# Optimization experiments

Hardware: AMD Instinct MI355X
Metric: run time of the kernel (lower is better)

The kernel has to match this reference:

```python
import jax, jax.numpy as jnp
import numpy as np

NUM_CODES = 8192
DIM = 512
COMMITMENT_COST = 0.25


def setup_inputs() -> dict:
    key = jax.random.key(0)
    kx, kc = jax.random.split(key)
    x = jax.random.normal(kx, (8, 4096, DIM), dtype=jnp.float32)
    # nn.init.uniform_(codebook.weight, -1/num_codes, 1/num_codes)
    bound = 1.0 / NUM_CODES
    codebook = jax.random.uniform(kc, (NUM_CODES, DIM), dtype=jnp.float32,
                                  minval=-bound, maxval=bound)
    return {"x": x, "codebook": codebook}


def reference(x, codebook):
    orig_shape = x.shape
    flat = x.reshape(-1, orig_shape[-1])              # [N, D]
    # Squared-distance expansion (argmin-equivalent to torch.cdist's L2):
    # ||f||^2 - 2 f.c + ||c||^2
    x_sq = jnp.sum(flat * flat, axis=-1, keepdims=True)          # [N, 1]
    c_sq = jnp.sum(codebook * codebook, axis=-1)                 # [K]
    dists = x_sq - 2.0 * jnp.einsum('nd,kd->nk', flat, codebook) + c_sq  # [N, K]
    indices_flat = jnp.argmin(dists, axis=-1)                    # [N] int
    quantized_flat = codebook[indices_flat]                      # [N, D]
    # codebook_loss = mse(quantized, sg(flat)); commitment = mse(flat, sg(quantized))
    codebook_loss = jnp.mean((quantized_flat - jax.lax.stop_gradient(flat)) ** 2)
    commitment_loss = jnp.mean((flat - jax.lax.stop_gradient(quantized_flat)) ** 2)
    vq_loss = codebook_loss + COMMITMENT_COST * commitment_loss
    # straight-through
    quantized_st = flat + jax.lax.stop_gradient(quantized_flat - flat)
    return (quantized_st.reshape(orig_shape), vq_loss,
            indices_flat.reshape(orig_shape[:-1]))
```

## Files before the change

kernel.cpp:

```cpp
#include <hip/hip_runtime.h>


#define NROWS 32768
#define KCODES 8192
#define DD 512
#define CAP 24
#define MARGIN 2.5e-4f

typedef __bf16 bf16_t;
typedef __bf16 bf16x4 __attribute__((ext_vector_type(4)));
typedef __bf16 bf16x8 __attribute__((ext_vector_type(8)));
typedef float f32x4 __attribute__((ext_vector_type(4)));

__device__ __forceinline__ int lofs(int row, int s) {
  return row * 32 + (((s ^ ((row >> 1) & 3))) << 3);
}

__device__ __forceinline__ void gld16(const bf16_t* g, bf16_t* l) {
  __builtin_amdgcn_global_load_lds(
      (const __attribute__((address_space(1))) void*)g,
      (__attribute__((address_space(3))) void*)l, 16, 0, 0);
}

__global__ __launch_bounds__(256) void sumsq_kernel(const float* __restrict__ in,
                                                    float* __restrict__ out,
                                                    int nrows) {
  const int wave = threadIdx.x >> 6;
  const int lane = threadIdx.x & 63;
  const int row = blockIdx.x * 4 + wave;
  if (row >= nrows) return;
  const float* p = in + (size_t)row * DD;
  double s = 0.0;
#pragma unroll
  for (int j = 0; j < DD / 64; ++j) {
    float v = p[j * 64 + lane];
    float sq = v * v;
    s += (double)sq;
  }
  for (int off = 32; off > 0; off >>= 1) s += __shfl_down(s, off, 64);
  if (lane == 0) out[row] = (float)s;
}

__global__ __launch_bounds__(256) void cvt_kernel(const float* __restrict__ in,
                                                  bf16_t* __restrict__ outb) {
  const int t = blockIdx.x * 256 + threadIdx.x;
  float4 v = *(const float4*)(in + (size_t)t * 4);
  bf16x4 o = {(bf16_t)v.x, (bf16_t)v.y, (bf16_t)v.z, (bf16_t)v.w};
  *(bf16x4*)(outb + (size_t)t * 4) = o;
}

__global__ __launch_bounds__(256, 2) void coarse_kernel(
    const bf16_t* __restrict__ xbf, const bf16_t* __restrict__ cbbf,
    const float* __restrict__ csq, int* __restrict__ cnt_g,
    int* __restrict__ list_g) {
  __shared__ bf16_t As[128 * 32];
  __shared__ bf16_t Bs[256 * 32];
  __shared__ unsigned long long best[128];
  __shared__ int cnt_l[128];
  __shared__ int list_l[128 * CAP];

  const int tid = threadIdx.x;
  const int w = tid >> 6;
  const int lane = tid & 63;
  const int q = lane >> 4;
  const int l15 = lane & 15;
  const int rOff = (w & 1) * 64;
  const int cOff = (w >> 1) * 128;
  const int row0 = blockIdx.x * 128;
  const int cbase = blockIdx.y * (KCODES / 2);

  for (int i = tid; i < 128; i += 256) { best[i] = ~0ULL; cnt_l[i] = 0; }

  const int sub = lane >> 2;
  const int pos = lane & 3;
  int arowc[2];
  const bf16_t *agp[2];
  bf16_t *alp[2];
#pragma unroll
  for (int a = 0; a < 2; ++a) {
    const int row = w * 32 + a * 16 + sub;
    const int sg = pos ^ ((row >> 1) & 3);
    arowc[a] = row;
    agp[a] = xbf + (size_t)(row0 + row) * DD + sg * 8;
    alp[a] = As + row * 32 + pos * 8;
  }
  const bf16_t *bgp[4];
  bf16_t *blp[4];
#pragma unroll
  for (int b = 0; b < 4; ++b) {
    const int row = w * 64 + b * 16 + sub;
    const int sg = pos ^ ((row >> 1) & 3);
    bgp[b] = cbbf + (size_t)(cbase + row) * DD + sg * 8;
    blp[b] = Bs + row * 32 + pos * 8;
  }

  int afofs[4], bfofs[8];
#pragma unroll
  for (int rt = 0; rt < 4; ++rt) afofs[rt] = lofs(rOff + rt * 16 + l15, q);
#pragma unroll
  for (int ct = 0; ct < 8; ++ct) bfofs[ct] = lofs(cOff + ct * 16 + l15, q);

  __syncthreads();

#pragma unroll 1
  for (int ci = 0; ci < (KCODES / 2) / 256; ++ci) {
    const int c0 = cbase + ci * 256;
    const size_t coff = (size_t)(ci * 256) * DD;
    f32x4 acc[4][8];
#pragma unroll
    for (int rt = 0; rt < 4; ++rt)
#pragma unroll
      for (int ct = 0; ct < 8; ++ct) {
        f32x4 z = {0.f, 0.f, 0.f, 0.f};
        acc[rt][ct] = z;
      }

#pragma unroll 1
    for (int kc = 0; kc < DD / 32; ++kc) {
      const int kb = kc * 32;
      __syncthreads();
      gld16(agp[0] + kb, alp[0]);
      gld16(agp[1] + kb, alp[1]);
#pragma unroll
      for (int b = 0; b < 4; ++b) gld16(bgp[b] + coff + kb, blp[b]);
      __syncthreads();

      bf16x8 af[4], bfr[8];
#pragma unroll
      for (int rt = 0; rt < 4; ++rt) af[rt] = *(const bf16x8*)&As[afofs[rt]];
#pragma unroll
      for (int ct = 0; ct < 8; ++ct) bfr[ct] = *(const bf16x8*)&Bs[bfofs[ct]];
#pragma unroll
      for (int rt = 0; rt < 4; ++rt)
#pragma unroll
        for (int ct = 0; ct < 8; ++ct)
          acc[rt][ct] = __builtin_amdgcn_mfma_f32_16x16x32_bf16(
              af[rt], bfr[ct], acc[rt][ct], 0, 0, 0);
    }

    float cs1[8];
#pragma unroll
    for (int ct = 0; ct < 8; ++ct)
      cs1[ct] = 1.0f + csq[c0 + cOff + ct * 16 + l15];

#pragma unroll
    for (int rt = 0; rt < 4; ++rt) {
#pragma unroll
      for (int reg = 0; reg < 4; ++reg) {
        unsigned long long pk = ~0ULL;
#pragma unroll
        for (int ct = 0; ct < 8; ++ct) {
          float d = fmaf(-2.0f, acc[rt][ct][reg], cs1[ct]);
          unsigned long long p =
              ((unsigned long long)__float_as_uint(d) << 32) |
              (unsigned)(c0 + cOff + ct * 16 + l15);
          if (p < pk) pk = p;
        }
#pragma unroll
        for (int m = 1; m <= 8; m <<= 1) {
          unsigned long long o = __shfl_xor(pk, m, 64);
          if (o < pk) pk = o;
        }
        if (l15 == 0) atomicMin(&best[rOff + rt * 16 + q * 4 + reg], pk);
      }
    }
    __syncthreads();

#pragma unroll
    for (int rt = 0; rt < 4; ++rt) {
#pragma unroll
      for (int reg = 0; reg < 4; ++reg) {
        const int rloc = rOff + rt * 16 + q * 4 + reg;
        const float thr = __uint_as_float((unsigned)(best[rloc] >> 32)) + MARGIN;
#pragma unroll
        for (int ct = 0; ct < 8; ++ct) {
          float d = fmaf(-2.0f, acc[rt][ct][reg], cs1[ct]);
          if (d <= thr) {
            int pos2 = atomicAdd(&cnt_l[rloc], 1);
            if (pos2 < CAP)
              list_l[rloc * CAP + pos2] = c0 + cOff + ct * 16 + l15;
          }
        }
      }
    }
    __syncthreads();
  }

  const int half = blockIdx.y;
  for (int i = tid; i < 128; i += 256) cnt_g[(row0 + i) * 2 + half] = cnt_l[i];
  for (int i = tid; i < 128 * CAP; i += 256) {
    const int r = i / CAP, p = i % CAP;
    list_g[((size_t)(row0 + r) * 2 + half) * CAP + p] = list_l[i];
  }
}

__global__ __launch_bounds__(256) void rescore_kernel(
    const float* __restrict__ x, const float* __restrict__ cb,
    const float* __restrict__ xsq, const float* __restrict__ csq,
    const int* __restrict__ list, const int* __restrict__ cnt,
    int* __restrict__ idxbuf) {
  const int row = blockIdx.x * 4 + (threadIdx.x >> 6);
  const int lane = threadIdx.x & 63;
  const int n0 = cnt[row * 2];
  const int n1 = cnt[row * 2 + 1];
  const float xs = xsq[row];
  const float4* xr4 = (const float4*)(x + (size_t)row * DD);
  unsigned long long bestv = ~0ULL;

  if (n0 >= 1 && n0 <= CAP && n1 >= 0 && n1 <= CAP && (n0 + n1) <= 56) {
    int myidx = -1;
    if (lane < n0) myidx = list[((size_t)row * 2) * CAP + lane];
    else if (lane - n0 < n1) myidx = list[((size_t)row * 2 + 1) * CAP + (lane - n0)];
    if (myidx >= 0) {
      const float4* cr4 = (const float4*)(cb + (size_t)myidx * DD);
      float acc = 0.0f;
      for (int k4 = 0; k4 < DD / 4; ++k4) {
        float4 xv = xr4[k4];
        float4 cv = cr4[k4];
        acc = fmaf(xv.x, cv.x, acc);
        acc = fmaf(xv.y, cv.y, acc);
        acc = fmaf(xv.z, cv.z, acc);
        acc = fmaf(xv.w, cv.w, acc);
      }
      float t = xs - 2.0f * acc;
      float d = t + csq[myidx];
      bestv = ((unsigned long long)__float_as_uint(d) << 32) | (unsigned)myidx;
    }
  } else {
    for (int idx = lane; idx < KCODES; idx += 64) {
      const float4* cr4 = (const float4*)(cb + (size_t)idx * DD);
      float acc = 0.0f;
      for (int k4 = 0; k4 < DD / 4; ++k4) {
        float4 xv = xr4[k4];
        float4 cv = cr4[k4];
        acc = fmaf(xv.x, cv.x, acc);
        acc = fmaf(xv.y, cv.y, acc);
        acc = fmaf(xv.z, cv.z, acc);
        acc = fmaf(xv.w, cv.w, acc);
      }
      float t = xs - 2.0f * acc;
      float d = t + csq[idx];
      unsigned long long pk =
          ((unsigned long long)__float_as_uint(d) << 32) | (unsigned)idx;
      if (pk < bestv) bestv = pk;
    }
  }
#pragma unroll
  for (int s = 1; s <= 32; s <<= 1) {
    unsigned long long o = __shfl_xor(bestv, s, 64);
    if (o < bestv) bestv = o;
  }
  if (lane == 0) idxbuf[row] = (int)(bestv & 0xffffffffu);
}

__global__ __launch_bounds__(128) void epilogue_kernel(
    const float* __restrict__ x, const float* __restrict__ cb,
    const int* __restrict__ idxbuf, float* __restrict__ out_q,
    float* __restrict__ out_idx_f, double* __restrict__ partials) {
  const int row = blockIdx.x;
  const int t = threadIdx.x;
  const int k = idxbuf[row];

  const float4* xr = (const float4*)(x + (size_t)row * DD);
  const float4* qr = (const float4*)(cb + (size_t)k * DD);
  float4* orow = (float4*)(out_q + (size_t)row * DD);

  float4 xv = xr[t];
  float4 qv = qr[t];
  float dx = qv.x - xv.x, dy = qv.y - xv.y, dz = qv.z - xv.z, dw = qv.w - xv.w;
  float4 o;
  o.x = xv.x + dx; o.y = xv.y + dy; o.z = xv.z + dz; o.w = xv.w + dw;
  orow[t] = o;

  float s0 = dx * dx, s1 = dy * dy, s2 = dz * dz, s3 = dw * dw;
  double part = (double)s0 + (double)s1 + (double)s2 + (double)s3;
  for (int off = 32; off > 0; off >>= 1) part += __shfl_down(part, off, 64);
  __shared__ double red[2];
  const int lane = t & 63, wv = t >> 6;
  if (lane == 0) red[wv] = part;
  __syncthreads();
  if (t == 0) {
    partials[row] = red[0] + red[1];
    out_idx_f[row] = (float)k;
  }
}

__global__ __launch_bounds__(256) void finalize_kernel(
    const double* __restrict__ partials, float* __restrict__ out_loss) {
  __shared__ double red[256];
  double s = 0.0;
  for (int i = threadIdx.x; i < NROWS; i += 256) s += partials[i];
  red[threadIdx.x] = s;
  __syncthreads();
  for (int st = 128; st > 0; st >>= 1) {
    if (threadIdx.x < st) red[threadIdx.x] += red[threadIdx.x + st];
    __syncthreads();
  }
  if (threadIdx.x == 0) {
    double mean = red[0] / ((double)NROWS * (double)DD);
    float cl = (float)mean;
    out_loss[0] = cl + 0.25f * cl;
  }
}

extern "C" void kernel_launch(void* const* d_in, const int* in_sizes, int n_in,
                              void* d_out, int out_size, void* d_ws,
                              size_t ws_size, hipStream_t stream) {
  const float* x = (const float*)d_in[0];
  const float* cb = (const float*)d_in[1];
  float* out = (float*)d_out;

  char* ws = (char*)d_ws;
  double* partials = (double*)ws;
  int* idxbuf = (int*)(ws + 262144);
  float* csq = (float*)(ws + 262144 + 131072);
  float* xsq = (float*)(ws + 262144 + 131072 + 32768);
  int* cnt = (int*)(ws + 262144 + 131072 + 32768 + 131072);
  int* list = (int*)(ws + 262144 + 131072 + 32768 + 131072 + 262144);

  bf16_t* cbbf = (bf16_t*)d_out;
  bf16_t* xbf = cbbf + (size_t)KCODES * DD;

  sumsq_kernel<<<KCODES / 4, 256, 0, stream>>>(cb, csq, KCODES);
  sumsq_kernel<<<NROWS / 4, 256, 0, stream>>>(x, xsq, NROWS);
  cvt_kernel<<<(KCODES * DD / 4) / 256, 256, 0, stream>>>(cb, cbbf);
  cvt_kernel<<<(NROWS * DD / 4) / 256, 256, 0, stream>>>(x, xbf);
  dim3 grid(NROWS / 128, 2);
  coarse_kernel<<<grid, 256, 0, stream>>>(xbf, cbbf, csq, cnt, list);
  rescore_kernel<<<NROWS / 4, 256, 0, stream>>>(x, cb, xsq, csq, list, cnt, idxbuf);
  epilogue_kernel<<<NROWS, 128, 0, stream>>>(x, cb, idxbuf, out,
                                             out + 16777216 + 1, partials);
  finalize_kernel<<<1, 256, 0, stream>>>(partials, out + 16777216);
}
```

Measured before the change: 1.063 ms.

## Fuse sumsq and bf16 convert, shrink coarse tile, remap blocks across XCDs

The separate sum-of-squares and bf16 conversion kernels are merged into one prep kernel, which removes two launches and a second read of the inputs. The coarse GEMM tile drops from 128x256 to 128x128 codes per iteration, cutting accumulator registers and LDS so occupancy can rise, at the cost of lower arithmetic intensity per LDS load. The 2D grid becomes a 1D grid whose block ids are remapped so that each XCD handles one codebook half and a contiguous set of row blocks, aiming for better L2 locality. The per-row minimum is now a 32-bit float reduction with no packed index, which is cheaper because only the threshold value is needed.

```diff
diff --git a/kernel.cpp b/kernel.cpp
--- a/kernel.cpp
+++ b/kernel.cpp
@@ -22,9 +22,10 @@
       (__attribute__((address_space(3))) void*)l, 16, 0, 0);
 }
 
-__global__ __launch_bounds__(256) void sumsq_kernel(const float* __restrict__ in,
-                                                    float* __restrict__ out,
-                                                    int nrows) {
+__global__ __launch_bounds__(256) void prep_kernel(const float* __restrict__ in,
+                                                   float* __restrict__ out_sq,
+                                                   bf16_t* __restrict__ outb,
+                                                   int nrows) {
   const int wave = threadIdx.x >> 6;
   const int lane = threadIdx.x & 63;
   const int row = blockIdx.x * 4 + wave;
@@ -38,15 +39,13 @@
     s += (double)sq;
   }
   for (int off = 32; off > 0; off >>= 1) s += __shfl_down(s, off, 64);
-  if (lane == 0) out[row] = (float)s;
-}
-
-__global__ __launch_bounds__(256) void cvt_kernel(const float* __restrict__ in,
-                                                  bf16_t* __restrict__ outb) {
-  const int t = blockIdx.x * 256 + threadIdx.x;
-  float4 v = *(const float4*)(in + (size_t)t * 4);
-  bf16x4 o = {(bf16_t)v.x, (bf16_t)v.y, (bf16_t)v.z, (bf16_t)v.w};
-  *(bf16x4*)(outb + (size_t)t * 4) = o;
+  if (lane == 0) out_sq[row] = (float)s;
+  const float4* p4 = (const float4*)p;
+  float4 a = p4[lane * 2];
+  float4 b = p4[lane * 2 + 1];
+  bf16x8 o = {(bf16_t)a.x, (bf16_t)a.y, (bf16_t)a.z, (bf16_t)a.w,
+              (bf16_t)b.x, (bf16_t)b.y, (bf16_t)b.z, (bf16_t)b.w};
+  *(bf16x8*)(outb + (size_t)row * DD + lane * 8) = o;
 }
 
 __global__ __launch_bounds__(256, 2) void coarse_kernel(
@@ -54,8 +53,8 @@
     const float* __restrict__ csq, int* __restrict__ cnt_g,
     int* __restrict__ list_g) {
   __shared__ bf16_t As[128 * 32];
-  __shared__ bf16_t Bs[256 * 32];
-  __shared__ unsigned long long best[128];
+  __shared__ bf16_t Bs[128 * 32];
+  __shared__ unsigned best[128];
   __shared__ int cnt_l[128];
   __shared__ int list_l[128 * CAP];
 
@@ -65,52 +64,49 @@
   const int q = lane >> 4;
   const int l15 = lane & 15;
   const int rOff = (w & 1) * 64;
-  const int cOff = (w >> 1) * 128;
-  const int row0 = blockIdx.x * 128;
-  const int cbase = blockIdx.y * (KCODES / 2);
-
-  for (int i = tid; i < 128; i += 256) { best[i] = ~0ULL; cnt_l[i] = 0; }
+  const int cOff = (w >> 1) * 64;
+
+  const int bid = blockIdx.x;
+  const int xcd = bid & 7;
+  const int g = bid >> 3;
+  const int half = xcd >> 2;
+  const int rowblk = (xcd & 3) * 64 + g;
+  const int row0 = rowblk * 128;
+  const int cbase = half * (KCODES / 2);
+
+  for (int i = tid; i < 128; i += 256) { best[i] = 0xFFFFFFFFu; cnt_l[i] = 0; }
 
   const int sub = lane >> 2;
   const int pos = lane & 3;
-  int arowc[2];
-  const bf16_t *agp[2];
-  bf16_t *alp[2];
+  const bf16_t *agp[2], *bgp[2];
+  bf16_t *alp[2], *blp[2];
 #pragma unroll
   for (int a = 0; a < 2; ++a) {
     const int row = w * 32 + a * 16 + sub;
     const int sg = pos ^ ((row >> 1) & 3);
-    arowc[a] = row;
     agp[a] = xbf + (size_t)(row0 + row) * DD + sg * 8;
     alp[a] = As + row * 32 + pos * 8;
-  }
-  const bf16_t *bgp[4];
-  bf16_t *blp[4];
-#pragma unroll
-  for (int b = 0; b < 4; ++b) {
-    const int row = w * 64 + b * 16 + sub;
-    const int sg = pos ^ ((row >> 1) & 3);
-    bgp[b] = cbbf + (size_t)(cbase + row) * DD + sg * 8;
-    blp[b] = Bs + row * 32 + pos * 8;
-  }
-
-  int afofs[4], bfofs[8];
+    bgp[a] = cbbf + (size_t)(cbase + row) * DD + sg * 8;
+    blp[a] = Bs + row * 32 + pos * 8;
+  }
+
+  int afofs[4], bfofs[4];
 #pragma unroll
   for (int rt = 0; rt < 4; ++rt) afofs[rt] = lofs(rOff + rt * 16 + l15, q);
 #pragma unroll
-  for (int ct = 0; ct < 8; ++ct) bfofs[ct] = lofs(cOff + ct * 16 + l15, q);
+  for (int ct = 0; ct < 4; ++ct) bfofs[ct] = lofs(cOff + ct * 16 + l15, q);
 
   __syncthreads();
 
 #pragma unroll 1
-  for (int ci = 0; ci < (KCODES / 2) / 256; ++ci) {
-    const int c0 = cbase + ci * 256;
-    const size_t coff = (size_t)(ci * 256) * DD;
-    f32x4 acc[4][8];
+  for (int ci = 0; ci < (KCODES / 2) / 128; ++ci) {
+    const int c0 = cbase + ci * 128;
+    const size_t coff = (size_t)(ci * 128) * DD;
+    f32x4 acc[4][4];
 #pragma unroll
     for (int rt = 0; rt < 4; ++rt)
 #pragma unroll
-      for (int ct = 0; ct < 8; ++ct) {
+      for (int ct = 0; ct < 4; ++ct) {
         f32x4 z = {0.f, 0.f, 0.f, 0.f};
         acc[rt][ct] = z;
       }
@@ -121,47 +117,45 @@
       __syncthreads();
       gld16(agp[0] + kb, alp[0]);
       gld16(agp[1] + kb, alp[1]);
-#pragma unroll
-      for (int b = 0; b < 4; ++b) gld16(bgp[b] + coff + kb, blp[b]);
+      gld16(bgp[0] + coff + kb, blp[0]);
+      gld16(bgp[1] + coff + kb, blp[1]);
       __syncthreads();
 
-      bf16x8 af[4], bfr[8];
+      bf16x8 af[4], bfr[4];
 #pragma unroll
       for (int rt = 0; rt < 4; ++rt) af[rt] = *(const bf16x8*)&As[afofs[rt]];
 #pragma unroll
-      for (int ct = 0; ct < 8; ++ct) bfr[ct] = *(const bf16x8*)&Bs[bfofs[ct]];
+      for (int ct = 0; ct < 4; ++ct) bfr[ct] = *(const bf16x8*)&Bs[bfofs[ct]];
 #pragma unroll
       for (int rt = 0; rt < 4; ++rt)
 #pragma unroll
-        for (int ct = 0; ct < 8; ++ct)
+        for (int ct = 0; ct < 4; ++ct)
           acc[rt][ct] = __builtin_amdgcn_mfma_f32_16x16x32_bf16(
               af[rt], bfr[ct], acc[rt][ct], 0, 0, 0);
     }
 
-    float cs1[8];
-#pragma unroll
-    for (int ct = 0; ct < 8; ++ct)
+    float cs1[4];
+#pragma unroll
+    for (int ct = 0; ct < 4; ++ct)
       cs1[ct] = 1.0f + csq[c0 + cOff + ct * 16 + l15];
 
 #pragma unroll
     for (int rt = 0; rt < 4; ++rt) {
 #pragma unroll
       for (int reg = 0; reg < 4; ++reg) {
-        unsigned long long pk = ~0ULL;
-#pragma unroll
-        for (int ct = 0; ct < 8; ++ct) {
+        float m = fmaf(-2.0f, acc[rt][0][reg], cs1[0]);
+#pragma unroll
+        for (int ct = 1; ct < 4; ++ct) {
           float d = fmaf(-2.0f, acc[rt][ct][reg], cs1[ct]);
-          unsigned long long p =
-              ((unsigned long long)__float_as_uint(d) << 32) |
-              (unsigned)(c0 + cOff + ct * 16 + l15);
-          if (p < pk) pk = p;
+          m = fminf(m, d);
         }
-#pragma unroll
-        for (int m = 1; m <= 8; m <<= 1) {
-          unsigned long long o = __shfl_xor(pk, m, 64);
-          if (o < pk) pk = o;
+        unsigned mb = __float_as_uint(m);
+#pragma unroll
+        for (int msk = 1; msk <= 8; msk <<= 1) {
+          unsigned o = __shfl_xor(mb, msk, 64);
+          mb = mb < o ? mb : o;
         }
-        if (l15 == 0) atomicMin(&best[rOff + rt * 16 + q * 4 + reg], pk);
+        if (l15 == 0) atomicMin(&best[rOff + rt * 16 + q * 4 + reg], mb);
       }
     }
     __syncthreads();
@@ -171,9 +165,9 @@
 #pragma unroll
       for (int reg = 0; reg < 4; ++reg) {
         const int rloc = rOff + rt * 16 + q * 4 + reg;
-        const float thr = __uint_as_float((unsigned)(best[rloc] >> 32)) + MARGIN;
-#pragma unroll
-        for (int ct = 0; ct < 8; ++ct) {
+        const float thr = __uint_as_float(best[rloc]) + MARGIN;
+#pragma unroll
+        for (int ct = 0; ct < 4; ++ct) {
           float d = fmaf(-2.0f, acc[rt][ct][reg], cs1[ct]);
           if (d <= thr) {
             int pos2 = atomicAdd(&cnt_l[rloc], 1);
@@ -186,7 +180,6 @@
     __syncthreads();
   }
 
-  const int half = blockIdx.y;
   for (int i = tid; i < 128; i += 256) cnt_g[(row0 + i) * 2 + half] = cnt_l[i];
   for (int i = tid; i < 128 * CAP; i += 256) {
     const int r = i / CAP, p = i % CAP;
@@ -321,12 +314,9 @@
   bf16_t* cbbf = (bf16_t*)d_out;
   bf16_t* xbf = cbbf + (size_t)KCODES * DD;
 
-  sumsq_kernel<<<KCODES / 4, 256, 0, stream>>>(cb, csq, KCODES);
-  sumsq_kernel<<<NROWS / 4, 256, 0, stream>>>(x, xsq, NROWS);
-  cvt_kernel<<<(KCODES * DD / 4) / 256, 256, 0, stream>>>(cb, cbbf);
-  cvt_kernel<<<(NROWS * DD / 4) / 256, 256, 0, stream>>>(x, xbf);
-  dim3 grid(NROWS / 128, 2);
-  coarse_kernel<<<grid, 256, 0, stream>>>(xbf, cbbf, csq, cnt, list);
+  prep_kernel<<<KCODES / 4, 256, 0, stream>>>(cb, csq, cbbf, KCODES);
+  prep_kernel<<<NROWS / 4, 256, 0, stream>>>(x, xsq, xbf, NROWS);
+  coarse_kernel<<<512, 256, 0, stream>>>(xbf, cbbf, csq, cnt, list);
   rescore_kernel<<<NROWS / 4, 256, 0, stream>>>(x, cb, xsq, csq, list, cnt, idxbuf);
   epilogue_kernel<<<NROWS, 128, 0, stream>>>(x, cb, idxbuf, out,
                                              out + 16777216 + 1, partials);
```

Result: faster. 948.1 us (-10.8%).
